# Kernel tuning notes

Measured on AMD Instinct MI355X. Metric: run time of the kernel, lower is better.

The kernel has to match this reference:

```python
import jax, jax.numpy as jnp
import numpy as np

H = 16
ROPE_BASE = 10000.0

def _rope_cos_sin(seq_len, d_k, dtype):
    inv_freq = 1.0 / (ROPE_BASE ** (jnp.arange(0, d_k, 2, dtype=jnp.float32) / d_k))
    t = jnp.arange(seq_len, dtype=jnp.float32)
    freqs = jnp.einsum('s,d->sd', t, inv_freq)          # [S, d_k/2]
    emb = jnp.concatenate([freqs, freqs], axis=-1)       # [S, d_k]
    return jnp.cos(emb).astype(dtype), jnp.sin(emb).astype(dtype)

def _rotate_half(x):
    x1, x2 = jnp.split(x, 2, axis=-1)
    return jnp.concatenate([-x2, x1], axis=-1)

def setup_inputs() -> dict:
    key = jax.random.key(0)
    ks = jax.random.split(key, 11)
    B, S, D = 2, 2048, 1024
    sc = 0.02
    return {
        'query': jax.random.normal(ks[0], (B, S, D), jnp.float32),
        'key':   jax.random.normal(ks[1], (B, S, D), jnp.float32),
        'value': jax.random.normal(ks[2], (B, S, D), jnp.float32),
        'Wq': jax.random.normal(ks[3], (D, D), jnp.float32) * sc,
        'bq': jnp.zeros((D,), jnp.float32),
        'Wk': jax.random.normal(ks[4], (D, D), jnp.float32) * sc,
        'bk': jnp.zeros((D,), jnp.float32),
        'Wv': jax.random.normal(ks[5], (D, D), jnp.float32) * sc,
        'bv': jnp.zeros((D,), jnp.float32),
        'Wo': jax.random.normal(ks[6], (D, D), jnp.float32) * sc,
        'bo': jnp.zeros((D,), jnp.float32),
    }

def reference(query, key, value, Wq, bq, Wk, bk, Wv, bv, Wo, bo):
    B, S, D = query.shape
    d_k = D // H
    # QKV projections (torch Linear: x @ W.T + b), split heads -> [B, H, S, d_k]
    def proj(x, W, b):
        return (x @ W.T + b).reshape(B, S, H, d_k).transpose(0, 2, 1, 3)
    q = proj(query, Wq, bq)
    k = proj(key, Wk, bk)
    v = proj(value, Wv, bv)
    # Rotary position embedding applied to q and k
    cos, sin = _rope_cos_sin(S, d_k, q.dtype)            # [S, d_k]
    cos = cos[None, None, :, :]
    sin = sin[None, None, :, :]
    q = q * cos + _rotate_half(q) * sin
    k = k * cos + _rotate_half(k) * sin
    # Scaled dot-product attention
    scores = jnp.einsum('bhqd,bhkd->bhqk', q, k) / jnp.sqrt(jnp.asarray(d_k, q.dtype))
    attn = jax.nn.softmax(scores, axis=-1)
    x = jnp.einsum('bhqk,bhkd->bhqd', attn, v)           # [B, H, S, d_k]
    x = x.transpose(0, 2, 1, 3).reshape(B, S, D)
    return x @ Wo.T + bo
```

## Files before the change

### kernel.cpp

```cpp
#include <hip/hip_runtime.h>
#include <hip/hip_bf16.h>
#include <math.h>


#define B_ 2
#define S_ 2048
#define D_ 1024
#define H_ 16
#define DK 64

typedef __attribute__((ext_vector_type(8)))  __bf16    bf16x8;
typedef __attribute__((ext_vector_type(8)))  _Float16  f16x8;
typedef __attribute__((ext_vector_type(4)))  float     f32x4;
typedef __attribute__((ext_vector_type(16))) float     f32x16;
typedef __attribute__((ext_vector_type(8)))  unsigned short u16x8;
typedef __attribute__((ext_vector_type(4)))  unsigned short u16x4;

#if __has_builtin(__builtin_amdgcn_exp2f)
#define EXP2(x) __builtin_amdgcn_exp2f(x)
#else
#define EXP2(x) exp2f(x)
#endif

static __device__ __forceinline__ unsigned short f2bf(float x) {
    union { float f; unsigned u; } v; v.f = x;
    unsigned r = v.u + 0x7FFFu + ((v.u >> 16) & 1u);
    return (unsigned short)(r >> 16);
}
static __device__ __forceinline__ unsigned cvtpk(float lo, float hi) {
    unsigned r;
    asm("v_cvt_pk_bf16_f32 %0, %1, %2" : "=v"(r) : "v"(lo), "v"(hi));
    return r;
}
static __device__ __forceinline__ unsigned cvtpk16(float lo, float hi) {
    unsigned r;
    asm("v_cvt_pkrtz_f16_f32 %0, %1, %2" : "=v"(r) : "v"(lo), "v"(hi));
    return r;
}
static __device__ __forceinline__ void gload_lds16(const void* g, void* l) {
    __builtin_amdgcn_global_load_lds(
        (const __attribute__((address_space(1))) void*)g,
        (__attribute__((address_space(3))) void*)l, 16, 0, 0);
}
static __device__ __forceinline__ int swz(int R, int c) {
    return ((R >> 1) << 6) + (((((R & 1) << 2) | c) ^ ((R >> 1) & 7)) << 3);
}

__global__ __launch_bounds__(256) void wsplit4(
    const float* __restrict__ W0, const float* __restrict__ W1,
    const float* __restrict__ W2, const float* __restrict__ W3,
    unsigned short* __restrict__ out)
{
    const int idx = blockIdx.x * 256 + threadIdx.x;
    const int t = idx >> 17;
    const size_t e = (size_t)(idx & 131071) * 8;
    const float* src = (t==0 ? W0 : t==1 ? W1 : t==2 ? W2 : W3) + e;
    float4 a = *(const float4*)src;
    float4 b = *(const float4*)(src + 4);
    float x[8] = {a.x,a.y,a.z,a.w,b.x,b.y,b.z,b.w};
    union { _Float16 h[8]; u16x8 v; } Hh;
    #pragma unroll
    for (int j = 0; j < 8; ++j) Hh.h[j] = (_Float16)x[j];
    *(u16x8*)(out + (size_t)t * 1048576 + e) = Hh.v;
}

__global__ __launch_bounds__(512) void trigemm(
    const float* __restrict__ Aq, const float* __restrict__ Ak,
    const float* __restrict__ Av, const unsigned short* __restrict__ wsp,
    const float* __restrict__ bq, const float* __restrict__ bk,
    const float* __restrict__ bv,
    unsigned short* __restrict__ qb, unsigned short* __restrict__ kb,
    unsigned short* __restrict__ vt)
{
    __shared__ __align__(16) char ldsb[32768];
    const int pid = blockIdx.z;
    const float* A    = (pid==0) ? Aq : (pid==1) ? Ak : Av;
    const float* bias = (pid==0) ? bq : (pid==1) ? bk : bv;
    const unsigned short* Whp = wsp + (size_t)pid * 1048576;

    const int tid = threadIdx.x;
    const int w = tid >> 6, lane = tid & 63;
    const int l15 = lane & 15, g4 = lane >> 4;
    const int wr = w >> 1, wc = w & 1;
    const int bx = blockIdx.x, by = blockIdx.y;

    const int arow = tid >> 2, ac = tid & 3;
    const float* gpA = A + (size_t)(bx*128 + arow) * 1024 + ac * 8;
    const int aoff = swz(arow, ac);

    const int sr_ = tid >> 3, slot_ = tid & 7;
    const int z_  = slot_ ^ (sr_ & 7);
    const int wR_ = sr_*2 + (z_ >> 2);
    const unsigned short* gpW = Whp + (size_t)(by*128 + wR_) * 1024 + (z_ & 3) * 8;

    f32x4 acc[2][4];
    #pragma unroll
    for (int m = 0; m < 2; ++m)
        #pragma unroll
        for (int n = 0; n < 4; ++n) acc[m][n] = (f32x4){0.f,0.f,0.f,0.f};

    {
        float4 p0 = *(const float4*)(gpA);
        float4 p1 = *(const float4*)(gpA + 4);
        gload_lds16(gpW, ldsb + 8192 + tid * 16);
        union { unsigned u[4]; u16x8 v; } hh;
        hh.u[0] = cvtpk16(p0.x, p0.y); hh.u[1] = cvtpk16(p0.z, p0.w);
        hh.u[2] = cvtpk16(p1.x, p1.y); hh.u[3] = cvtpk16(p1.z, p1.w);
        *(u16x8*)((unsigned short*)ldsb + aoff) = hh.v;
    }
    asm volatile("s_waitcnt vmcnt(0) lgkmcnt(0)" ::: "memory");
    __builtin_amdgcn_s_barrier();
    asm volatile("" ::: "memory");

    for (int t = 0; t < 32; ++t) {
        const int cur = t & 1;
        float4 n0, n1;
        if (t < 31) {
            n0 = *(const float4*)(gpA + (t+1)*32);
            n1 = *(const float4*)(gpA + (t+1)*32 + 4);
            gload_lds16(gpW + (size_t)(t+1)*32, ldsb + (cur^1)*16384 + 8192 + tid*16);
            asm volatile("s_waitcnt vmcnt(3)" ::: "memory");
        } else {
            asm volatile("s_waitcnt vmcnt(0)" ::: "memory");
        }
        __builtin_amdgcn_s_barrier();
        asm volatile("" ::: "memory");

        const unsigned short* Ab = (const unsigned short*)(ldsb + cur*16384);
        const unsigned short* Wb = Ab + 4096;
        f16x8 ah[2], wh4[4];
        #pragma unroll
        for (int m = 0; m < 2; ++m)
            ah[m] = *(const f16x8*)(Ab + swz(wr*32 + m*16 + l15, g4));
        #pragma unroll
        for (int n = 0; n < 4; ++n)
            wh4[n] = *(const f16x8*)(Wb + swz(wc*64 + n*16 + l15, g4));
        #pragma unroll
        for (int m = 0; m < 2; ++m)
            #pragma unroll
            for (int n = 0; n < 4; ++n)
                acc[m][n] = __builtin_amdgcn_mfma_f32_16x16x32_f16(ah[m], wh4[n], acc[m][n], 0,0,0);

        if (t < 31) {
            union { unsigned u[4]; u16x8 v; } hh;
            hh.u[0] = cvtpk16(n0.x, n0.y); hh.u[1] = cvtpk16(n0.z, n0.w);
            hh.u[2] = cvtpk16(n1.x, n1.y); hh.u[3] = cvtpk16(n1.z, n1.w);
            *(u16x8*)((unsigned short*)(ldsb + (cur^1)*16384) + aoff) = hh.v;
        }
        asm volatile("s_waitcnt lgkmcnt(0)" ::: "memory");
        __builtin_amdgcn_s_barrier();
        asm volatile("" ::: "memory");
    }

    const int colBase = by*128 + wc*64;
    const int rowBase = bx*128 + wr*32;
    const int h = colBase >> 6;

    if (pid < 2) {
        unsigned short* Out = pid ? kb : qb;
        const float QSC = pid ? 1.0f : 0.125f * 1.44269504088896340736f;
        #pragma unroll
        for (int m = 0; m < 2; ++m) {
            const int srow0 = rowBase + m*16 + g4*4;
            const int b = srow0 >> 11;
            unsigned short* hb2 = Out + (size_t)(b*H_ + h) * S_ * DK;
            #pragma unroll
            for (int n = 0; n < 2; ++n) {
                const int d = n*16 + l15;
                const float invf = exp2f((float)d * -0.4152410118609203f);
                const float b1 = bias[h*64 + d], b2 = bias[h*64 + d + 32];
                #pragma unroll
                for (int r = 0; r < 4; ++r) {
                    const int s = (srow0 + r) & 2047;
                    const float x1 = acc[m][n][r]   + b1;
                    const float x2 = acc[m][n+2][r] + b2;
                    float sn, cc;
                    __sincosf((float)s * invf, &sn, &cc);
                    const float o1 = (x1*cc - x2*sn) * QSC;
                    const float o2 = (x2*cc + x1*sn) * QSC;
                    if (pid == 0) {
                        unsigned short* dst = hb2 + (size_t)s * DK;
                        dst[d]      = f2bf(o1);
                        dst[d + 32] = f2bf(o2);
                    } else {
                        unsigned short* tb = hb2 + (s >> 6) * 4096 + (s & 63) * 8;
                        tb[(d >> 3) * 512 + (d & 7)]        = f2bf(o1);
                        tb[(d >> 3) * 512 + 2048 + (d & 7)] = f2bf(o2);
                    }
                }
            }
        }
    } else {
        #pragma unroll
        for (int m = 0; m < 2; ++m) {
            const int srow0 = rowBase + m*16 + g4*4;
            const int b = srow0 >> 11, s0 = srow0 & 2047;
            unsigned short* tb = vt + (size_t)(b*H_ + h) * S_ * DK
                               + (s0 >> 6) * 4096 + ((s0 & 63) >> 3) * 512 + (s0 & 7);
            #pragma unroll
            for (int n = 0; n < 4; ++n) {
                const int d = n*16 + l15;
                const float bb = bias[h*64 + d];
                u16x4 pk;
                #pragma unroll
                for (int r = 0; r < 4; ++r) pk[r] = f2bf(acc[m][n][r] + bb);
                *(u16x4*)(tb + d * 8) = pk;
            }
        }
    }
}

__global__ __launch_bounds__(512, 1) void attn_mfma8(
    const unsigned short* __restrict__ Qb, const unsigned short* __restrict__ Kb,
    const unsigned short* __restrict__ Vt, unsigned short* __restrict__ Xh)
{
    __shared__ __align__(16) char lds[65536];
    const unsigned bid = blockIdx.x;
    const int xcd = bid & 7, idx = bid >> 3;
    const int bh  = xcd * 4 + (idx >> 3);
    const int qt  = idx & 7;
    const int tid = threadIdx.x;
    const int w = tid >> 6, lane = tid & 63;
    const int l31 = lane & 31, hi = lane >> 5;
    const size_t bhO = (size_t)bh * S_ * DK;
    const int q0 = qt * 256 + w * 32;

    const int u0   = w * 4;
    const int isV  = u0 >> 4;
    const int u15  = u0 & 15;
    const int su0  = u15 >> 3;
    const unsigned short* sb = (isV ? Vt : Kb) + bhO;
    const int ch0 = u15 & 7;
    char* const dbase = lds;

    bf16x8 qf[4];
    #pragma unroll
    for (int ks = 0; ks < 4; ++ks)
        qf[ks] = *(const bf16x8*)(Qb + bhO + (size_t)(q0 + l31) * DK + ks*16 + hi*8);

    f32x16 oT[2];
    #pragma unroll
    for (int dh = 0; dh < 2; ++dh)
        #pragma unroll
        for (int r = 0; r < 16; ++r) oT[dh][r] = 0.f;
    float l_ = 0.f;

    #define ASTAGE(T, BUF) do {                                                     \
        const unsigned short* g_ = sb + (size_t)((T)*2 + su0) * 4096 + ch0 * 512    \
                                   + lane * 8;                                      \
        char* d_ = dbase + (BUF)*32768 + isV*16384 + su0*8192 + ch0*1024 + lane*16; \
        gload_lds16(g_,         d_);                                                \
        gload_lds16(g_ + 512,   d_ + 1024);                                         \
        gload_lds16(g_ + 1024,  d_ + 2048);                                         \
        gload_lds16(g_ + 1536,  d_ + 3072);                                         \
    } while (0)

    ASTAGE(0, 0);
    asm volatile("s_waitcnt vmcnt(0)" ::: "memory");
    __builtin_amdgcn_s_barrier();
    asm volatile("" ::: "memory");

    for (int t = 0; t < 16; ++t) {
        const int cur = t & 1;
        if (t < 15) {
            ASTAGE(t + 1, cur ^ 1);
            asm volatile("s_waitcnt vmcnt(4)" ::: "memory");
        } else {
            asm volatile("s_waitcnt vmcnt(0)" ::: "memory");
        }
        __builtin_amdgcn_s_barrier();
        asm volatile("" ::: "memory");

        const char* Kl = lds + cur * 32768;
        const char* Vl = Kl + 16384;

        f32x16 s2[4];
        __builtin_amdgcn_s_setprio(1);
        #pragma unroll
        for (int kb2 = 0; kb2 < 4; ++kb2) {
            f32x16 a;
            #pragma unroll
            for (int r = 0; r < 16; ++r) a[r] = 0.f;
            const char* kbase = Kl + (kb2 >> 1) * 8192 + ((kb2 & 1) * 32 + l31) * 16;
            #pragma unroll
            for (int ks = 0; ks < 4; ++ks) {
                bf16x8 kf = *(const bf16x8*)(kbase + (ks*2 + hi) * 1024);
                a = __builtin_amdgcn_mfma_f32_32x32x16_bf16(kf, qf[ks], a, 0, 0, 0);
            }
            s2[kb2] = a;
        }
        __builtin_amdgcn_s_setprio(0);

        {
            float lsum = 0.f;
            #pragma unroll
            for (int kb2 = 0; kb2 < 4; ++kb2)
                #pragma unroll
                for (int r = 0; r < 16; ++r) {
                    const float p = EXP2(s2[kb2][r]);
                    s2[kb2][r] = p; lsum += p;
                }
            l_ += lsum;
        }

        #pragma unroll
        for (int ks2 = 0; ks2 < 8; ++ks2) {
            const int kb2 = ks2 >> 1;
            const int R0  = (ks2 & 1) * 8;
            unsigned a0 = cvtpk(s2[kb2][R0+0], s2[kb2][R0+1]);
            unsigned a1 = cvtpk(s2[kb2][R0+2], s2[kb2][R0+3]);
            unsigned b0 = cvtpk(s2[kb2][R0+4], s2[kb2][R0+5]);
            unsigned b1 = cvtpk(s2[kb2][R0+6], s2[kb2][R0+7]);
            asm("v_permlane32_swap_b32 %0, %1" : "+v"(a0), "+v"(b0));
            asm("v_permlane32_swap_b32 %0, %1" : "+v"(a1), "+v"(b1));
            union { unsigned u[4]; bf16x8 v; } pf;
            pf.u[0] = a0; pf.u[1] = a1; pf.u[2] = b0; pf.u[3] = b1;
            const char* vbase = Vl + (ks2 >> 2) * 8192 + (((ks2 & 3) * 2) + hi) * 1024;
            __builtin_amdgcn_s_setprio(1);
            #pragma unroll
            for (int dh = 0; dh < 2; ++dh) {
                bf16x8 vf = *(const bf16x8*)(vbase + (dh*32 + l31) * 16);
                oT[dh] = __builtin_amdgcn_mfma_f32_32x32x16_bf16(vf, pf.v, oT[dh], 0, 0, 0);
            }
            __builtin_amdgcn_s_setprio(0);
        }

        asm volatile("" ::: "memory");
        __builtin_amdgcn_s_barrier();
        asm volatile("" ::: "memory");
    }
    #undef ASTAGE

    l_ += __shfl_xor(l_, 32, 64);
    const float inv = 1.0f / l_;
    const int b = bh >> 4, h = bh & 15;
    const int q = q0 + l31;
    unsigned short* xh = Xh + (((size_t)b * S_ + q) * H_ + h) * DK;
    #pragma unroll
    for (int dh = 0; dh < 2; ++dh)
        #pragma unroll
        for (int tt = 0; tt < 4; ++tt) {
            const int dk0 = dh*32 + tt*8 + hi*4;
            union { _Float16 hh[4]; u16x4 v; } o;
            #pragma unroll
            for (int r = 0; r < 4; ++r)
                o.hh[r] = (_Float16)(oT[dh][tt*4 + r] * inv);
            *(u16x4*)(xh + dk0) = o.v;
        }
}

__global__ __launch_bounds__(512) void mfma_gemm0(
    const unsigned short* __restrict__ Ah, const unsigned short* __restrict__ Wh,
    const float* __restrict__ bias, float* __restrict__ Out)
{
    __shared__ __align__(16) char ldsb[32768];
    const int tid = threadIdx.x;
    const int w = tid >> 6, lane = tid & 63;
    const int l15 = lane & 15, g4 = lane >> 4;
    const int wr = w >> 1, wc = w & 1;
    const int bx = blockIdx.x, by = blockIdx.y;

    const int ten = (w >> 1) & 1, qq = w & 1;
    const unsigned short* gsrc = ten ? Wh : Ah;
    const int row0 = ten ? by * 128 : bx * 128;
    const int lr8 = lane >> 3;
    const int zz  = (lane & 7) ^ lr8;
    const int wR0 = qq*64 + (lr8 << 1) + (zz >> 2);
    const unsigned short* gp0 = gsrc + (size_t)(row0 + wR0) * 1024 + (zz & 3) * 8;

    f32x4 acc[2][4];
    #pragma unroll
    for (int m = 0; m < 2; ++m)
        #pragma unroll
        for (int n = 0; n < 4; ++n) acc[m][n] = (f32x4){0.f,0.f,0.f,0.f};

    #define STAGE(T, BUF) do {                                              \
        if (w < 4) {                                                        \
            const unsigned short* g_ = gp0 + (size_t)(T) * 32;              \
            char* d_ = ldsb + (BUF)*16384 + ten*8192 + qq*4096;             \
            gload_lds16(g_,          d_);                                   \
            gload_lds16(g_ + 16384,  d_ + 1024);                            \
            gload_lds16(g_ + 32768,  d_ + 2048);                            \
            gload_lds16(g_ + 49152,  d_ + 3072);                            \
        }                                                                   \
    } while (0)

    STAGE(0, 0);
    asm volatile("s_waitcnt vmcnt(0)" ::: "memory");
    __builtin_amdgcn_s_barrier();
    asm volatile("" ::: "memory");

    for (int t = 0; t < 32; ++t) {
        const int cur = t & 1;
        if (t < 31) {
            STAGE(t + 1, cur ^ 1);
            asm volatile("s_waitcnt vmcnt(4)" ::: "memory");
        } else {
            asm volatile("s_waitcnt vmcnt(0)" ::: "memory");
        }
        __builtin_amdgcn_s_barrier();
        asm volatile("" ::: "memory");

        const unsigned short* Ahb = (const unsigned short*)(ldsb + cur*16384);
        const unsigned short* Whb = Ahb + 4096;
        f16x8 ah2[2], wh4[4];
        #pragma unroll
        for (int m = 0; m < 2; ++m)
            ah2[m] = *(const f16x8*)(Ahb + swz(wr*32 + m*16 + l15, g4));
        #pragma unroll
        for (int n = 0; n < 4; ++n)
            wh4[n] = *(const f16x8*)(Whb + swz(wc*64 + n*16 + l15, g4));
        #pragma unroll
        for (int m = 0; m < 2; ++m)
            #pragma unroll
            for (int n = 0; n < 4; ++n)
                acc[m][n] = __builtin_amdgcn_mfma_f32_16x16x32_f16(ah2[m], wh4[n], acc[m][n], 0,0,0);

        asm volatile("" ::: "memory");
        __builtin_amdgcn_s_barrier();
        asm volatile("" ::: "memory");
    }
    #undef STAGE

    const int colBase = by*128 + wc*64;
    const int rowBase = bx*128 + wr*32;
    #pragma unroll
    for (int m = 0; m < 2; ++m) {
        const int row = rowBase + m*16 + g4*4;
        #pragma unroll
        for (int n = 0; n < 4; ++n) {
            const int col = colBase + n*16 + l15;
            const float bb = bias[col];
            #pragma unroll
            for (int r = 0; r < 4; ++r)
                Out[(size_t)(row + r) * 1024 + col] = acc[m][n][r] + bb;
        }
    }
}

extern "C" void kernel_launch(void* const* d_in, const int* in_sizes, int n_in,
                              void* d_out, int out_size, void* d_ws, size_t ws_size,
                              hipStream_t stream)
{
    const float* query = (const float*)d_in[0];
    const float* key   = (const float*)d_in[1];
    const float* value = (const float*)d_in[2];
    const float* Wq = (const float*)d_in[3];  const float* bq = (const float*)d_in[4];
    const float* Wk = (const float*)d_in[5];  const float* bk = (const float*)d_in[6];
    const float* Wv = (const float*)d_in[7];  const float* bv = (const float*)d_in[8];
    const float* Wo = (const float*)d_in[9];  const float* bo = (const float*)d_in[10];
    float* out = (float*)d_out;

    char* ws = (char*)d_ws;
    const size_t MB = (size_t)1 << 20;
    unsigned short* Xh  = (unsigned short*)(ws + 0*MB);
    unsigned short* qb  = (unsigned short*)(ws + 16*MB);
    unsigned short* vt  = (unsigned short*)(ws + 24*MB);
    unsigned short* kb  = (unsigned short*)(ws + 40*MB);
    unsigned short* wsp = (unsigned short*)(ws + 48*MB);
    unsigned short* Woh = wsp + 3145728;

    wsplit4<<<2048, 256, 0, stream>>>(Wq, Wk, Wv, Wo, wsp);

    trigemm<<<dim3(32, 8, 3), 512, 0, stream>>>(query, key, value, wsp,
                                                bq, bk, bv, qb, kb, vt);

    attn_mfma8<<<256, 512, 0, stream>>>(qb, kb, vt, Xh);

    mfma_gemm0<<<dim3(32, 8), 512, 0, stream>>>(Xh, Woh, bo, out);
}
```

Baseline: 108.4 us.

## Fuse fp32-to-fp16 weight conversion into projection GEMMs and drop wsplit4 kernel

Removes the separate weight-conversion kernel. The QKV and output GEMMs now load fp32 weights directly, convert them to fp16 in registers and store them to LDS, in place of the async global_load_lds path. This saves one kernel launch plus the write and re-read of the converted weights. In exchange, each weight tile is converted many times, once per row block (32 times), and the weight loads double in bytes. The GEMM loops also change from async LDS loads to a register-staged prefetch.

```diff
diff --git a/kernel.cpp b/kernel.cpp
--- a/kernel.cpp
+++ b/kernel.cpp
@@ -45,28 +45,26 @@
 static __device__ __forceinline__ int swz(int R, int c) {
     return ((R >> 1) << 6) + (((((R & 1) << 2) | c) ^ ((R >> 1) & 7)) << 3);
 }
-
-__global__ __launch_bounds__(256) void wsplit4(
-    const float* __restrict__ W0, const float* __restrict__ W1,
-    const float* __restrict__ W2, const float* __restrict__ W3,
-    unsigned short* __restrict__ out)
-{
-    const int idx = blockIdx.x * 256 + threadIdx.x;
-    const int t = idx >> 17;
-    const size_t e = (size_t)(idx & 131071) * 8;
-    const float* src = (t==0 ? W0 : t==1 ? W1 : t==2 ? W2 : W3) + e;
-    float4 a = *(const float4*)src;
-    float4 b = *(const float4*)(src + 4);
-    float x[8] = {a.x,a.y,a.z,a.w,b.x,b.y,b.z,b.w};
-    union { _Float16 h[8]; u16x8 v; } Hh;
-    #pragma unroll
-    for (int j = 0; j < 8; ++j) Hh.h[j] = (_Float16)x[j];
-    *(u16x8*)(out + (size_t)t * 1048576 + e) = Hh.v;
+static __device__ __forceinline__ u16x8 packA(float4 a, float4 b) {
+    union { unsigned u[4]; u16x8 v; } hh;
+    hh.u[0] = cvtpk16(a.x, a.y); hh.u[1] = cvtpk16(a.z, a.w);
+    hh.u[2] = cvtpk16(b.x, b.y); hh.u[3] = cvtpk16(b.z, b.w);
+    return hh.v;
+}
+static __device__ __forceinline__ u16x8 packW(float4 a, float4 b) {
+    union { _Float16 h[8]; u16x8 v; } hh;
+    hh.h[0]=(_Float16)a.x; hh.h[1]=(_Float16)a.y;
+    hh.h[2]=(_Float16)a.z; hh.h[3]=(_Float16)a.w;
+    hh.h[4]=(_Float16)b.x; hh.h[5]=(_Float16)b.y;
+    hh.h[6]=(_Float16)b.z; hh.h[7]=(_Float16)b.w;
+    return hh.v;
 }
 
 __global__ __launch_bounds__(512) void trigemm(
     const float* __restrict__ Aq, const float* __restrict__ Ak,
-    const float* __restrict__ Av, const unsigned short* __restrict__ wsp,
+    const float* __restrict__ Av,
+    const float* __restrict__ Wq, const float* __restrict__ Wk,
+    const float* __restrict__ Wv,
     const float* __restrict__ bq, const float* __restrict__ bk,
     const float* __restrict__ bv,
     unsigned short* __restrict__ qb, unsigned short* __restrict__ kb,
@@ -75,8 +73,8 @@
     __shared__ __align__(16) char ldsb[32768];
     const int pid = blockIdx.z;
     const float* A    = (pid==0) ? Aq : (pid==1) ? Ak : Av;
+    const float* W    = (pid==0) ? Wq : (pid==1) ? Wk : Wv;
     const float* bias = (pid==0) ? bq : (pid==1) ? bk : bv;
-    const unsigned short* Whp = wsp + (size_t)pid * 1048576;
 
     const int tid = threadIdx.x;
     const int w = tid >> 6, lane = tid & 63;
@@ -86,12 +84,9 @@
 
     const int arow = tid >> 2, ac = tid & 3;
     const float* gpA = A + (size_t)(bx*128 + arow) * 1024 + ac * 8;
+    const float* gpW = W + (size_t)(by*128 + arow) * 1024 + ac * 8;
     const int aoff = swz(arow, ac);
-
-    const int sr_ = tid >> 3, slot_ = tid & 7;
-    const int z_  = slot_ ^ (sr_ & 7);
-    const int wR_ = sr_*2 + (z_ >> 2);
-    const unsigned short* gpW = Whp + (size_t)(by*128 + wR_) * 1024 + (z_ & 3) * 8;
+    const int woff = 4096 + aoff;
 
     f32x4 acc[2][4];
     #pragma unroll
@@ -100,31 +95,26 @@
         for (int n = 0; n < 4; ++n) acc[m][n] = (f32x4){0.f,0.f,0.f,0.f};
 
     {
-        float4 p0 = *(const float4*)(gpA);
-        float4 p1 = *(const float4*)(gpA + 4);
-        gload_lds16(gpW, ldsb + 8192 + tid * 16);
-        union { unsigned u[4]; u16x8 v; } hh;
-        hh.u[0] = cvtpk16(p0.x, p0.y); hh.u[1] = cvtpk16(p0.z, p0.w);
-        hh.u[2] = cvtpk16(p1.x, p1.y); hh.u[3] = cvtpk16(p1.z, p1.w);
-        *(u16x8*)((unsigned short*)ldsb + aoff) = hh.v;
-    }
-    asm volatile("s_waitcnt vmcnt(0) lgkmcnt(0)" ::: "memory");
+        float4 a0 = *(const float4*)(gpA);
+        float4 a1 = *(const float4*)(gpA + 4);
+        float4 w0 = *(const float4*)(gpW);
+        float4 w1 = *(const float4*)(gpW + 4);
+        *(u16x8*)((unsigned short*)ldsb + aoff) = packA(a0, a1);
+        *(u16x8*)((unsigned short*)ldsb + woff) = packW(w0, w1);
+    }
+    asm volatile("s_waitcnt lgkmcnt(0)" ::: "memory");
     __builtin_amdgcn_s_barrier();
     asm volatile("" ::: "memory");
 
     for (int t = 0; t < 32; ++t) {
         const int cur = t & 1;
-        float4 n0, n1;
+        float4 na0, na1, nw0, nw1;
         if (t < 31) {
-            n0 = *(const float4*)(gpA + (t+1)*32);
-            n1 = *(const float4*)(gpA + (t+1)*32 + 4);
-            gload_lds16(gpW + (size_t)(t+1)*32, ldsb + (cur^1)*16384 + 8192 + tid*16);
-            asm volatile("s_waitcnt vmcnt(3)" ::: "memory");
-        } else {
-            asm volatile("s_waitcnt vmcnt(0)" ::: "memory");
-        }
-        __builtin_amdgcn_s_barrier();
-        asm volatile("" ::: "memory");
+            na0 = *(const float4*)(gpA + (size_t)(t+1)*32);
+            na1 = *(const float4*)(gpA + (size_t)(t+1)*32 + 4);
+            nw0 = *(const float4*)(gpW + (size_t)(t+1)*32);
+            nw1 = *(const float4*)(gpW + (size_t)(t+1)*32 + 4);
+        }
 
         const unsigned short* Ab = (const unsigned short*)(ldsb + cur*16384);
         const unsigned short* Wb = Ab + 4096;
@@ -142,10 +132,9 @@
                 acc[m][n] = __builtin_amdgcn_mfma_f32_16x16x32_f16(ah[m], wh4[n], acc[m][n], 0,0,0);
 
         if (t < 31) {
-            union { unsigned u[4]; u16x8 v; } hh;
-            hh.u[0] = cvtpk16(n0.x, n0.y); hh.u[1] = cvtpk16(n0.z, n0.w);
-            hh.u[2] = cvtpk16(n1.x, n1.y); hh.u[3] = cvtpk16(n1.z, n1.w);
-            *(u16x8*)((unsigned short*)(ldsb + (cur^1)*16384) + aoff) = hh.v;
+            unsigned short* nb = (unsigned short*)(ldsb + (cur^1)*16384);
+            *(u16x8*)(nb + aoff) = packA(na0, na1);
+            *(u16x8*)(nb + woff) = packW(nw0, nw1);
         }
         asm volatile("s_waitcnt lgkmcnt(0)" ::: "memory");
         __builtin_amdgcn_s_barrier();
@@ -350,7 +339,7 @@
 }
 
 __global__ __launch_bounds__(512) void mfma_gemm0(
-    const unsigned short* __restrict__ Ah, const unsigned short* __restrict__ Wh,
+    const unsigned short* __restrict__ Xh, const float* __restrict__ Wo,
     const float* __restrict__ bias, float* __restrict__ Out)
 {
     __shared__ __align__(16) char ldsb[32768];
@@ -360,13 +349,11 @@
     const int wr = w >> 1, wc = w & 1;
     const int bx = blockIdx.x, by = blockIdx.y;
 
-    const int ten = (w >> 1) & 1, qq = w & 1;
-    const unsigned short* gsrc = ten ? Wh : Ah;
-    const int row0 = ten ? by * 128 : bx * 128;
-    const int lr8 = lane >> 3;
-    const int zz  = (lane & 7) ^ lr8;
-    const int wR0 = qq*64 + (lr8 << 1) + (zz >> 2);
-    const unsigned short* gp0 = gsrc + (size_t)(row0 + wR0) * 1024 + (zz & 3) * 8;
+    const int arow = tid >> 2, ac = tid & 3;
+    const unsigned short* gpX = Xh + (size_t)(bx*128 + arow) * 1024 + ac * 8;
+    const float*          gpW = Wo + (size_t)(by*128 + arow) * 1024 + ac * 8;
+    const int aoff = swz(arow, ac);
+    const int woff = 4096 + aoff;
 
     f32x4 acc[2][4];
     #pragma unroll
@@ -374,53 +361,51 @@
         #pragma unroll
         for (int n = 0; n < 4; ++n) acc[m][n] = (f32x4){0.f,0.f,0.f,0.f};
 
-    #define STAGE(T, BUF) do {                                              \
-        if (w < 4) {                                                        \
-            const unsigned short* g_ = gp0 + (size_t)(T) * 32;              \
-            char* d_ = ldsb + (BUF)*16384 + ten*8192 + qq*4096;             \
-            gload_lds16(g_,          d_);                                   \
-            gload_lds16(g_ + 16384,  d_ + 1024);                            \
-            gload_lds16(g_ + 32768,  d_ + 2048);                            \
-            gload_lds16(g_ + 49152,  d_ + 3072);                            \
-        }                                                                   \
-    } while (0)
-
-    STAGE(0, 0);
-    asm volatile("s_waitcnt vmcnt(0)" ::: "memory");
+    {
+        u16x8  x0 = *(const u16x8*)(gpX);
+        float4 w0 = *(const float4*)(gpW);
+        float4 w1 = *(const float4*)(gpW + 4);
+        *(u16x8*)((unsigned short*)ldsb + aoff) = x0;
+        *(u16x8*)((unsigned short*)ldsb + woff) = packW(w0, w1);
+    }
+    asm volatile("s_waitcnt lgkmcnt(0)" ::: "memory");
     __builtin_amdgcn_s_barrier();
     asm volatile("" ::: "memory");
 
     for (int t = 0; t < 32; ++t) {
         const int cur = t & 1;
+        u16x8  nx0;
+        float4 nw0, nw1;
         if (t < 31) {
-            STAGE(t + 1, cur ^ 1);
-            asm volatile("s_waitcnt vmcnt(4)" ::: "memory");
-        } else {
-            asm volatile("s_waitcnt vmcnt(0)" ::: "memory");
-        }
+            nx0 = *(const u16x8*)(gpX + (size_t)(t+1)*32);
+            nw0 = *(const float4*)(gpW + (size_t)(t+1)*32);
+            nw1 = *(const float4*)(gpW + (size_t)(t+1)*32 + 4);
+        }
+
+        const unsigned short* Ab = (const unsigned short*)(ldsb + cur*16384);
+        const unsigned short* Wb = Ab + 4096;
+        f16x8 ah2[2], wh4[4];
+        #pragma unroll
+        for (int m = 0; m < 2; ++m)
+            ah2[m] = *(const f16x8*)(Ab + swz(wr*32 + m*16 + l15, g4));
+        #pragma unroll
+        for (int n = 0; n < 4; ++n)
+            wh4[n] = *(const f16x8*)(Wb + swz(wc*64 + n*16 + l15, g4));
+        #pragma unroll
+        for (int m = 0; m < 2; ++m)
+            #pragma unroll
+            for (int n = 0; n < 4; ++n)
+                acc[m][n] = __builtin_amdgcn_mfma_f32_16x16x32_f16(ah2[m], wh4[n], acc[m][n], 0,0,0);
+
+        if (t < 31) {
+            unsigned short* nb = (unsigned short*)(ldsb + (cur^1)*16384);
+            *(u16x8*)(nb + aoff) = nx0;
+            *(u16x8*)(nb + woff) = packW(nw0, nw1);
+        }
+        asm volatile("s_waitcnt lgkmcnt(0)" ::: "memory");
         __builtin_amdgcn_s_barrier();
         asm volatile("" ::: "memory");
-
-        const unsigned short* Ahb = (const unsigned short*)(ldsb + cur*16384);
-        const unsigned short* Whb = Ahb + 4096;
-        f16x8 ah2[2], wh4[4];
-        #pragma unroll
-        for (int m = 0; m < 2; ++m)
-            ah2[m] = *(const f16x8*)(Ahb + swz(wr*32 + m*16 + l15, g4));
-        #pragma unroll
-        for (int n = 0; n < 4; ++n)
-            wh4[n] = *(const f16x8*)(Whb + swz(wc*64 + n*16 + l15, g4));
-        #pragma unroll
-        for (int m = 0; m < 2; ++m)
-            #pragma unroll
-            for (int n = 0; n < 4; ++n)
-                acc[m][n] = __builtin_amdgcn_mfma_f32_16x16x32_f16(ah2[m], wh4[n], acc[m][n], 0,0,0);
-
-        asm volatile("" ::: "memory");
-        __builtin_amdgcn_s_barrier();
-        asm volatile("" ::: "memory");
-    }
-    #undef STAGE
+    }
 
     const int colBase = by*128 + wc*64;
     const int rowBase = bx*128 + wr*32;
@@ -457,15 +442,11 @@
     unsigned short* qb  = (unsigned short*)(ws + 16*MB);
     unsigned short* vt  = (unsigned short*)(ws + 24*MB);
     unsigned short* kb  = (unsigned short*)(ws + 40*MB);
-    unsigned short* wsp = (unsigned short*)(ws + 48*MB);
-    unsigned short* Woh = wsp + 3145728;
-
-    wsplit4<<<2048, 256, 0, stream>>>(Wq, Wk, Wv, Wo, wsp);
-
-    trigemm<<<dim3(32, 8, 3), 512, 0, stream>>>(query, key, value, wsp,
+
+    trigemm<<<dim3(32, 8, 3), 512, 0, stream>>>(query, key, value, Wq, Wk, Wv,
                                                 bq, bk, bv, qb, kb, vt);
 
     attn_mfma8<<<256, 512, 0, stream>>>(qb, kb, vt, Xh);
 
-    mfma_gemm0<<<dim3(32, 8), 512, 0, stream>>>(Xh, Woh, bo, out);
-}
+    mfma_gemm0<<<dim3(32, 8), 512, 0, stream>>>(Xh, Wo, bo, out);
+}
```

Measured after the change: 134.8 us. +24.4%, slower.
